# Performance work log

Hardware: AMD Instinct MI355X
Metric: run time of the kernel (lower is better)

Reference implementation:

```python
import jax, jax.numpy as jnp
import numpy as np

N = 50000
E = 800000
IN_C = 16
H = 64
EA = 3
L = 3
EPS = 1e-5

def layer_norm(h, g, b):
    mu = jnp.mean(h, axis=-1, keepdims=True)
    var = jnp.var(h, axis=-1, keepdims=True)
    return (h - mu) * jax.lax.rsqrt(var + EPS) * g + b

def setup_inputs() -> dict:
    key = jax.random.key(0)
    ks = jax.random.split(key, 24)
    s = lambda *sh: 0.05
    d = {}
    d["x"] = jax.random.normal(ks[0], (N, IN_C), jnp.float32)
    d["edge_index"] = jax.random.randint(ks[1], (2, E), 0, N, jnp.int32)
    d["edge_attr"] = jax.random.normal(ks[2], (E, EA), jnp.float32)
    # encoder
    d["enc_w"] = jax.random.normal(ks[3], (IN_C, H), jnp.float32) * 0.1
    d["enc_b"] = jnp.zeros((H,), jnp.float32)
    d["enc_ln_g"] = jnp.ones((H,), jnp.float32)
    d["enc_ln_b"] = jnp.zeros((H,), jnp.float32)
    # message-passing MLPs (stacked over layers)
    d["mlp_w1"] = jax.random.normal(ks[4], (L, H + EA, H // 2), jnp.float32) * 0.1
    d["mlp_b1"] = jnp.zeros((L, H // 2), jnp.float32)
    d["mlp_w2"] = jax.random.normal(ks[5], (L, H // 2, H), jnp.float32) * 0.1
    d["mlp_b2"] = jnp.zeros((L, H), jnp.float32)
    d["ln_g"] = jnp.ones((L, H), jnp.float32)
    d["ln_b"] = jnp.zeros((L, H), jnp.float32)
    # heads
    d["depth_w1"] = jax.random.normal(ks[6], (H, H // 2), jnp.float32) * 0.1
    d["depth_b1"] = jnp.zeros((H // 2,), jnp.float32)
    d["depth_w2"] = jax.random.normal(ks[7], (H // 2, 1), jnp.float32) * 0.1
    d["depth_b2"] = jnp.zeros((1,), jnp.float32)
    d["vel_w1"] = jax.random.normal(ks[8], (H, H // 2), jnp.float32) * 0.1
    d["vel_b1"] = jnp.zeros((H // 2,), jnp.float32)
    d["vel_w2"] = jax.random.normal(ks[9], (H // 2, 2), jnp.float32) * 0.1
    d["vel_b2"] = jnp.zeros((2,), jnp.float32)
    return d

def reference(x, edge_index, edge_attr, enc_w, enc_b, enc_ln_g, enc_ln_b,
              mlp_w1, mlp_b1, mlp_w2, mlp_b2, ln_g, ln_b,
              depth_w1, depth_b1, depth_w2, depth_b2,
              vel_w1, vel_b1, vel_w2, vel_b2):
    src, dst = edge_index[0], edge_index[1]  # PyG: x_j = x[src], aggregate at dst
    # encoder (dropout inactive in eval mode)
    h = layer_norm(x @ enc_w + enc_b, enc_ln_g, enc_ln_b)
    h = jax.nn.relu(h)
    # in-degree counts for mean aggregation (isolated nodes -> 0, like PyG)
    cnt = jax.ops.segment_sum(jnp.ones((E,), jnp.float32), dst, num_segments=N)
    inv_cnt = jnp.where(cnt > 0, 1.0 / jnp.maximum(cnt, 1.0), 0.0)[:, None]
    for i in range(L):
        m_in = jnp.concatenate([h[src], edge_attr], axis=1)          # [E, H+EA]
        m = jax.nn.relu(m_in @ mlp_w1[i] + mlp_b1[i]) @ mlp_w2[i] + mlp_b2[i]  # [E, H]
        agg = jax.ops.segment_sum(m, dst, num_segments=N) * inv_cnt  # mean aggregate
        h = layer_norm(h + agg, ln_g[i], ln_b[i])
    depth = jax.nn.relu(h @ depth_w1 + depth_b1) @ depth_w2 + depth_b2    # [N,1]
    velocity = jax.nn.relu(h @ vel_w1 + vel_b1) @ vel_w2 + vel_b2         # [N,2]
    return (depth, velocity)
```

## Files before the change

kernel.cpp:

```cpp
#include <hip/hip_runtime.h>
#include <hip/hip_bf16.h>

typedef __hip_bfloat16 bf16;
typedef unsigned int u32;
typedef float f4v __attribute__((ext_vector_type(4)));

#define NN 50000
#define NE 800000
#define INC 16
#define HD 64
#define EPSV 1e-5f
#define NB1 196

__device__ __forceinline__ float b2f(bf16 v) { return __bfloat162float(v); }
__device__ __forceinline__ bool is_bf(const void* det) {
  return *(const u32*)det == 0x3F803F80u;
}

__device__ __forceinline__ float4 ldnt4(const float4* p) {
  f4v t = __builtin_nontemporal_load(reinterpret_cast<const f4v*>(p));
  float4 r; r.x = t[0]; r.y = t[1]; r.z = t[2]; r.w = t[3];
  return r;
}

template<typename T> __device__ __forceinline__ float ldv(const T* p, int i);
template<> __device__ __forceinline__ float ldv<float>(const float* p, int i) { return p[i]; }
template<> __device__ __forceinline__ float ldv<bf16>(const bf16* p, int i) { return b2f(p[i]); }

#define W1F   0
#define B1F   6432
#define W2F   6528
#define B2F   12672
#define DW1F  12864
#define DB1F  14912
#define DW2F  14944
#define DB2F  14976
#define VW1F  14977
#define VB1F  17025
#define VW2F  17057
#define VB2F  17121
#define WFTOT 17123

#define H_OFF    0
#define P0_OFF   3200000
#define CSR_OFF  4800000
#define WF_OFF   8000000
#define CNTI_OFF (WF_OFF + WFTOT)
#define RS_OFF   (CNTI_OFF + NN)
#define BSUM_OFF (RS_OFF + NN)
#define BOFF_OFF (BSUM_OFF + 256)
#define LPOS_OFF (BOFF_OFF + 256)
#define INV_OFF  (LPOS_OFF + NE)
#define P1_OFF   (INV_OFF + NE)
#define WS_NEED_ROOMY ((size_t)(P1_OFF + NN * 32) * 4)

template<typename T>
__device__ __forceinline__ void prep_body(
    const T* w1, const T* b1, const T* w2, const T* b2,
    const T* dw1, const T* db1, const T* dw2, const T* db2,
    const T* vw1, const T* vb1, const T* vw2, const T* vb2,
    float* wf, int i) {
  float v;
  if      (i < B1F)  v = ldv(w1,  i - W1F);
  else if (i < W2F)  v = ldv(b1,  i - B1F);
  else if (i < B2F)  v = ldv(w2,  i - W2F);
  else if (i < DW1F) v = ldv(b2,  i - B2F);
  else if (i < DB1F) v = ldv(dw1, i - DW1F);
  else if (i < DW2F) v = ldv(db1, i - DB1F);
  else if (i < DB2F) v = ldv(dw2, i - DW2F);
  else if (i < VW1F) v = ldv(db2, i - DB2F);
  else if (i < VB1F) v = ldv(vw1, i - VW1F);
  else if (i < VW2F) v = ldv(vb1, i - VB1F);
  else if (i < VB2F) v = ldv(vw2, i - VW2F);
  else               v = ldv(vb2, i - VB2F);
  wf[i] = v;
}

__global__ __launch_bounds__(256) void prep_kernel(
    const void* w1, const void* b1, const void* w2, const void* b2,
    const void* dw1, const void* db1, const void* dw2, const void* db2,
    const void* vw1, const void* vb1, const void* vw2, const void* vb2,
    float* __restrict__ wf, const void* __restrict__ det) {
  int i = blockIdx.x * blockDim.x + threadIdx.x;
  if (i >= WFTOT) return;
  if (is_bf(det))
    prep_body((const bf16*)w1, (const bf16*)b1, (const bf16*)w2, (const bf16*)b2,
              (const bf16*)dw1, (const bf16*)db1, (const bf16*)dw2, (const bf16*)db2,
              (const bf16*)vw1, (const bf16*)vb1, (const bf16*)vw2, (const bf16*)vb2, wf, i);
  else
    prep_body((const float*)w1, (const float*)b1, (const float*)w2, (const float*)b2,
              (const float*)dw1, (const float*)db1, (const float*)dw2, (const float*)db2,
              (const float*)vw1, (const float*)vb1, (const float*)vw2, (const float*)vb2, wf, i);
}

__global__ __launch_bounds__(256) void encoder_kernel(
    const void* __restrict__ x, const void* __restrict__ enc_w,
    const void* __restrict__ enc_b, const void* __restrict__ g,
    const void* __restrict__ b, float* __restrict__ h,
    float* __restrict__ pout, const float* __restrict__ nw1,
    const float* __restrict__ nb1, const void* __restrict__ det) {
  __shared__ float shv[4][64];
  int node = (blockIdx.x * blockDim.x + threadIdx.x) >> 6;
  int lane = threadIdx.x & 63;
  int w = threadIdx.x >> 6;
  if (node >= NN) return;
  int jl = lane & 31, half = lane >> 5;
  float xv[INC], wv[INC], ebv, gv, bv;
  if (is_bf(det)) {
    const bf16* xp = (const bf16*)x + node * INC;
    const bf16* wp = (const bf16*)enc_w;
    #pragma unroll
    for (int k = 0; k < INC; k++) { xv[k] = b2f(xp[k]); wv[k] = b2f(wp[k * HD + lane]); }
    ebv = b2f(((const bf16*)enc_b)[lane]);
    gv  = b2f(((const bf16*)g)[lane]);
    bv  = b2f(((const bf16*)b)[lane]);
  } else {
    const float* xp = (const float*)x + node * INC;
    const float* wp = (const float*)enc_w;
    #pragma unroll
    for (int k = 0; k < INC; k++) { xv[k] = xp[k]; wv[k] = wp[k * HD + lane]; }
    ebv = ((const float*)enc_b)[lane];
    gv  = ((const float*)g)[lane];
    bv  = ((const float*)b)[lane];
  }
  float acc = ebv;
  #pragma unroll
  for (int k = 0; k < INC; k++) acc += xv[k] * wv[k];
  float s1 = acc, s2 = acc * acc;
  #pragma unroll
  for (int o = 32; o; o >>= 1) { s1 += __shfl_xor(s1, o); s2 += __shfl_xor(s2, o); }
  float mu = s1 * (1.0f / 64.0f);
  float var = fmaxf(s2 * (1.0f / 64.0f) - mu * mu, 0.0f);
  float d = acc - mu;
  float hv = fmaxf(d * rsqrtf(var + EPSV) * gv + bv, 0.0f);
  h[node * HD + lane] = hv;
  shv[w][lane] = hv;
  float pacc = 0.0f;
  int kb = half << 5;
  #pragma unroll
  for (int k4 = 0; k4 < 32; k4 += 4) {
    float4 h4 = *reinterpret_cast<const float4*>(&shv[w][kb + k4]);
    int kk = kb + k4;
    pacc += h4.x * nw1[kk * 32 + jl] + h4.y * nw1[(kk + 1) * 32 + jl]
          + h4.z * nw1[(kk + 2) * 32 + jl] + h4.w * nw1[(kk + 3) * 32 + jl];
  }
  pacc += __shfl_xor(pacc, 32);
  if (half == 0) pout[node * 32 + jl] = pacc + nb1[jl];
}

__global__ __launch_bounds__(256) void count_kernel(const int* __restrict__ ei,
                                                    int* __restrict__ cnt,
                                                    int* __restrict__ lpos) {
  int e = blockIdx.x * blockDim.x + threadIdx.x;
  if (e < NE) lpos[e] = atomicAdd(&cnt[ei[NE + e]], 1);
}

__global__ __launch_bounds__(256) void scan1_kernel(const int* __restrict__ cnt,
                                                    int* __restrict__ ex,
                                                    int* __restrict__ bsum) {
  __shared__ int s[256];
  int t = threadIdx.x, idx = blockIdx.x * 256 + t;
  int v = (idx < NN) ? cnt[idx] : 0;
  s[t] = v;
  __syncthreads();
  #pragma unroll
  for (int off = 1; off < 256; off <<= 1) {
    int u = (t >= off) ? s[t - off] : 0;
    __syncthreads();
    s[t] += u;
    __syncthreads();
  }
  if (idx < NN) ex[idx] = s[t] - v;
  if (t == 255) bsum[blockIdx.x] = s[255];
}

__global__ __launch_bounds__(256) void scan2_kernel(int* __restrict__ bsum,
                                                    int* __restrict__ boff) {
  __shared__ int s[256];
  int t = threadIdx.x;
  int v = (t < NB1) ? bsum[t] : 0;
  s[t] = v;
  __syncthreads();
  #pragma unroll
  for (int off = 1; off < 256; off <<= 1) {
    int u = (t >= off) ? s[t - off] : 0;
    __syncthreads();
    s[t] += u;
    __syncthreads();
  }
  boff[t] = s[t] - v;
}

__global__ __launch_bounds__(256) void scan3_kernel(int* __restrict__ rs,
                                                    const int* __restrict__ boff) {
  int idx = blockIdx.x * 256 + threadIdx.x;
  if (idx >= NN) return;
  rs[idx] += boff[blockIdx.x];
}

__global__ __launch_bounds__(256) void inv_kernel(const int* __restrict__ ei,
                                                  const int* __restrict__ rs,
                                                  const int* __restrict__ lpos,
                                                  int* __restrict__ inv) {
  int e = blockIdx.x * blockDim.x + threadIdx.x;
  if (e >= NE) return;
  int dst = ei[NE + e];
  inv[rs[dst] + lpos[e]] = e;
}

__global__ __launch_bounds__(256) void fill_kernel(const int* __restrict__ inv,
                                                   const int* __restrict__ ei,
                                                   const void* __restrict__ attr,
                                                   float4* __restrict__ csr,
                                                   const void* __restrict__ det) {
  int p = blockIdx.x * blockDim.x + threadIdx.x;
  if (p >= NE) return;
  int e = inv[p];
  int src = ei[e];
  float a0, a1, a2;
  if (is_bf(det)) {
    const bf16* ap = (const bf16*)attr + 3 * e;
    a0 = b2f(ap[0]); a1 = b2f(ap[1]); a2 = b2f(ap[2]);
  } else {
    const float* ap = (const float*)attr + 3 * e;
    a0 = ap[0]; a1 = ap[1]; a2 = ap[2];
  }
  float4 v; v.x = a0; v.y = a1; v.z = a2; v.w = __int_as_float(src);
  csr[p] = v;
}

__global__ __launch_bounds__(256) void node_pre_kernel(
    const float* __restrict__ h, const float* __restrict__ w1,
    const float* __restrict__ b1, float* __restrict__ p) {
  int t = blockIdx.x * blockDim.x + threadIdx.x;
  int node = t >> 5;
  int j = t & 31;
  if (node >= NN) return;
  const float* hr = h + node * HD;
  float acc = b1[j];
  #pragma unroll
  for (int k = 0; k < HD; k++) acc += hr[k] * w1[k * 32 + j];
  p[node * 32 + j] = acc;
}

__global__ __launch_bounds__(128) void gather_kernel(
    float* __restrict__ h, const float* __restrict__ pin,
    float* __restrict__ pnext, const float4* __restrict__ csr,
    const int* __restrict__ rs, const int* __restrict__ cnt,
    const float* __restrict__ w1a, const float* __restrict__ w2,
    const float* __restrict__ b2v, const void* __restrict__ gbase,
    const void* __restrict__ bbase, int layer,
    const float* __restrict__ nw1, const float* __restrict__ nb1,
    int do_pnext, const float* __restrict__ wf, void* __restrict__ out,
    const void* __restrict__ det) {
  __shared__ float sacc[2][2][32];
  __shared__ float shv[2][2][64];
  int wid = (blockIdx.x * blockDim.x + threadIdx.x) >> 6;
  int lane = threadIdx.x & 63;
  int w = threadIdx.x >> 6;
  int n0 = 2 * wid, n1 = 2 * wid + 1;
  if (n0 >= NN) return;
  int jl = lane & 31, half = lane >> 5;
  float wa0 = w1a[jl], wa1 = w1a[32 + jl], wa2 = w1a[64 + jl];
  int s0 = rs[n0], c0 = cnt[n0];
  int s1 = rs[n1], c1 = cnt[n1];
  float hres0 = h[n0 * HD + lane];
  float hres1 = h[n1 * HD + lane];
  float b2l = b2v[lane];

  bool isbf = is_bf(det);
  int gidx = layer * HD + lane;
  float gv, bv;
  if (isbf) {
    gv = b2f(((const bf16*)gbase)[gidx]);
    bv = b2f(((const bf16*)bbase)[gidx]);
  } else {
    gv = ((const float*)gbase)[gidx];
    bv = ((const float*)bbase)[gidx];
  }

  int cm10 = (c0 > 0) ? c0 - 1 : 0;
  int cm11 = (c1 > 0) ? c1 - 1 : 0;
  int t0 = (c0 > 0) ? s0 : 0;
  int t1 = (c1 > 0) ? s1 : 0;

  float acc0 = 0.0f, acc1 = 0.0f;
  int cmax = max(c0, c1);
  if (cmax > 0) {
    float4 ed0[8], ed1[8];
    #pragma unroll
    for (int t = 0; t < 8; t++) {
      ed0[t] = ldnt4(&csr[t0 + min(2 * t + half, cm10)]);
      ed1[t] = ldnt4(&csr[t1 + min(2 * t + half, cm11)]);
    }
    for (int b0 = 0; b0 < cmax; b0 += 16) {
      float q0[8], q1[8];
      #pragma unroll
      for (int t = 0; t < 8; t++) q0[t] = pin[__float_as_int(ed0[t].w) * 32 + jl];
      #pragma unroll
      for (int t = 0; t < 8; t++) q1[t] = pin[__float_as_int(ed1[t].w) * 32 + jl];
      float pa0[8], pa1[8];
      #pragma unroll
      for (int t = 0; t < 8; t++)
        pa0[t] = ed0[t].x * wa0 + ed0[t].y * wa1 + ed0[t].z * wa2;
      #pragma unroll
      for (int t = 0; t < 8; t++)
        pa1[t] = ed1[t].x * wa0 + ed1[t].y * wa1 + ed1[t].z * wa2;
      int nb = b0 + 16;
      if (nb < cmax) {
        #pragma unroll
        for (int t = 0; t < 8; t++) {
          ed0[t] = ldnt4(&csr[t0 + min(nb + 2 * t + half, cm10)]);
          ed1[t] = ldnt4(&csr[t1 + min(nb + 2 * t + half, cm11)]);
        }
      }
      #pragma unroll
      for (int t = 0; t < 8; t++) {
        int eoff = b0 + 2 * t + half;
        float r0v = fmaxf(q0[t] + pa0[t], 0.0f);
        acc0 += (eoff < c0) ? r0v : 0.0f;
        float r1v = fmaxf(q1[t] + pa1[t], 0.0f);
        acc1 += (eoff < c1) ? r1v : 0.0f;
      }
    }
  }
  acc0 += __shfl_xor(acc0, 32);
  acc1 += __shfl_xor(acc1, 32);

  if (half == 0) { sacc[w][0][jl] = acc0; sacc[w][1][jl] = acc1; }
  float m0 = 0.0f, m1 = 0.0f;
  #pragma unroll
  for (int j4 = 0; j4 < 32; j4 += 4) {
    float4 a0 = *reinterpret_cast<const float4*>(&sacc[w][0][j4]);
    float4 a1 = *reinterpret_cast<const float4*>(&sacc[w][1][j4]);
    float w20 = w2[(j4 + 0) * HD + lane], w21 = w2[(j4 + 1) * HD + lane];
    float w22 = w2[(j4 + 2) * HD + lane], w23 = w2[(j4 + 3) * HD + lane];
    m0 += a0.x * w20 + a0.y * w21 + a0.z * w22 + a0.w * w23;
    m1 += a1.x * w20 + a1.y * w21 + a1.z * w22 + a1.w * w23;
  }
  float aggv0 = (c0 > 0) ? (m0 / (float)c0 + b2l) : 0.0f;
  float aggv1 = (c1 > 0) ? (m1 / (float)c1 + b2l) : 0.0f;

  float v0 = hres0 + aggv0, v1 = hres1 + aggv1;
  float s10 = v0, s20 = v0 * v0, s11 = v1, s21 = v1 * v1;
  #pragma unroll
  for (int o = 32; o; o >>= 1) {
    s10 += __shfl_xor(s10, o); s20 += __shfl_xor(s20, o);
    s11 += __shfl_xor(s11, o); s21 += __shfl_xor(s21, o);
  }
  float mu0 = s10 * (1.0f / 64.0f), mu1 = s11 * (1.0f / 64.0f);
  float var0 = fmaxf(s20 * (1.0f / 64.0f) - mu0 * mu0, 0.0f);
  float var1 = fmaxf(s21 * (1.0f / 64.0f) - mu1 * mu1, 0.0f);
  float hv0 = (v0 - mu0) * rsqrtf(var0 + EPSV) * gv + bv;
  float hv1 = (v1 - mu1) * rsqrtf(var1 + EPSV) * gv + bv;

  shv[w][0][lane] = hv0;
  shv[w][1][lane] = hv1;

  if (do_pnext) {
    float p0a = 0.0f, p1a = 0.0f;
    int kb = half << 5;
    #pragma unroll
    for (int k4 = 0; k4 < 32; k4 += 4) {
      float4 h0 = *reinterpret_cast<const float4*>(&shv[w][0][kb + k4]);
      float4 h1 = *reinterpret_cast<const float4*>(&shv[w][1][kb + k4]);
      int kk = kb + k4;
      float n0v = nw1[kk * 32 + jl], n1v = nw1[(kk + 1) * 32 + jl];
      float n2v = nw1[(kk + 2) * 32 + jl], n3v = nw1[(kk + 3) * 32 + jl];
      p0a += h0.x * n0v + h0.y * n1v + h0.z * n2v + h0.w * n3v;
      p1a += h1.x * n0v + h1.y * n1v + h1.z * n2v + h1.w * n3v;
    }
    p0a += __shfl_xor(p0a, 32);
    p1a += __shfl_xor(p1a, 32);
    if (half == 0) {
      pnext[n0 * 32 + jl] = p0a + nb1[jl];
      pnext[n1 * 32 + jl] = p1a + nb1[jl];
    }
  }

  if (layer == 2) {
    const float* w1h = wf + (half ? VW1F : DW1F);
    float a20 = half ? wf[VB1F + jl] : wf[DB1F + jl];
    float a21 = a20;
    #pragma unroll
    for (int k4 = 0; k4 < 64; k4 += 4) {
      float4 h0 = *reinterpret_cast<const float4*>(&shv[w][0][k4]);
      float4 h1 = *reinterpret_cast<const float4*>(&shv[w][1][k4]);
      float wv0 = w1h[(k4 + 0) * 32 + jl], wv1 = w1h[(k4 + 1) * 32 + jl];
      float wv2 = w1h[(k4 + 2) * 32 + jl], wv3 = w1h[(k4 + 3) * 32 + jl];
      a20 += h0.x * wv0 + h0.y * wv1 + h0.z * wv2 + h0.w * wv3;
      a21 += h1.x * wv0 + h1.y * wv1 + h1.z * wv2 + h1.w * wv3;
    }
    a20 = fmaxf(a20, 0.0f);
    a21 = fmaxf(a21, 0.0f);
    float r00, r10, r01, r11;
    if (half == 0) {
      r00 = a20 * wf[DW2F + jl]; r10 = 0.0f;
      r01 = a21 * wf[DW2F + jl]; r11 = 0.0f;
    } else {
      r00 = a20 * wf[VW2F + 2 * jl]; r10 = a20 * wf[VW2F + 2 * jl + 1];
      r01 = a21 * wf[VW2F + 2 * jl]; r11 = a21 * wf[VW2F + 2 * jl + 1];
    }
    #pragma unroll
    for (int o = 16; o; o >>= 1) {
      r00 += __shfl_xor(r00, o); r10 += __shfl_xor(r10, o);
      r01 += __shfl_xor(r01, o); r11 += __shfl_xor(r11, o);
    }
    if (lane == 0) {
      float d0 = r00 + wf[DB2F];
      float d1 = r01 + wf[DB2F];
      if (isbf) {
        ((bf16*)out)[n0] = __float2bfloat16(d0);
        ((bf16*)out)[n1] = __float2bfloat16(d1);
      } else {
        ((float*)out)[n0] = d0;
        ((float*)out)[n1] = d1;
      }
    }
    if (lane == 32) {
      float v00 = r00 + wf[VB2F], v01 = r10 + wf[VB2F + 1];
      float v10 = r01 + wf[VB2F], v11 = r11 + wf[VB2F + 1];
      if (isbf) {
        ((bf16*)out)[NN + 2 * n0]     = __float2bfloat16(v00);
        ((bf16*)out)[NN + 2 * n0 + 1] = __float2bfloat16(v01);
        ((bf16*)out)[NN + 2 * n1]     = __float2bfloat16(v10);
        ((bf16*)out)[NN + 2 * n1 + 1] = __float2bfloat16(v11);
      } else {
        ((float*)out)[NN + 2 * n0]     = v00;
        ((float*)out)[NN + 2 * n0 + 1] = v01;
        ((float*)out)[NN + 2 * n1]     = v10;
        ((float*)out)[NN + 2 * n1 + 1] = v11;
      }
    }
  } else {
    h[n0 * HD + lane] = hv0;
    h[n1 * HD + lane] = hv1;
  }
}

extern "C" void kernel_launch(void* const* d_in, const int* in_sizes, int n_in,
                              void* d_out, int out_size, void* d_ws, size_t ws_size,
                              hipStream_t stream) {
  const void* x     = d_in[0];
  const int*  ei    = (const int*)d_in[1];
  const void* attr  = d_in[2];
  const void* enc_w = d_in[3];
  const void* enc_b = d_in[4];
  const void* enc_g = d_in[5];
  const void* enc_bb= d_in[6];
  const void* mw1   = d_in[7];
  const void* mb1   = d_in[8];
  const void* mw2   = d_in[9];
  const void* mb2   = d_in[10];
  const void* lng   = d_in[11];
  const void* lnb   = d_in[12];
  const void* dw1   = d_in[13];
  const void* db1   = d_in[14];
  const void* dw2   = d_in[15];
  const void* db2   = d_in[16];
  const void* vw1   = d_in[17];
  const void* vb1   = d_in[18];
  const void* vw2   = d_in[19];
  const void* vb2   = d_in[20];

  float* ws    = (float*)d_ws;
  float* h     = ws + H_OFF;
  float* p0    = ws + P0_OFF;
  float4* csr  = (float4*)(ws + CSR_OFF);
  float* wf    = ws + WF_OFF;
  int*   cnti  = (int*)(ws + CNTI_OFF);
  int*   rs    = (int*)(ws + RS_OFF);
  int*   bsum  = (int*)(ws + BSUM_OFF);
  int*   boff  = (int*)(ws + BOFF_OFF);
  int*   lpos  = (int*)(ws + LPOS_OFF);
  int*   inv   = (int*)(ws + INV_OFF);
  float* p1    = ws + P1_OFF;
  bool roomy = ws_size >= WS_NEED_ROOMY;

  hipMemsetAsync(cnti, 0, (size_t)NN * sizeof(int), stream);
  prep_kernel<<<(WFTOT + 255) / 256, 256, 0, stream>>>(
      mw1, mb1, mw2, mb2, dw1, db1, dw2, db2, vw1, vb1, vw2, vb2, wf, enc_g);
  encoder_kernel<<<(NN + 3) / 4, 256, 0, stream>>>(
      x, enc_w, enc_b, enc_g, enc_bb, h, p0, wf + W1F, wf + B1F, enc_g);
  count_kernel<<<(NE + 255) / 256, 256, 0, stream>>>(ei, cnti, lpos);
  scan1_kernel<<<NB1, 256, 0, stream>>>(cnti, rs, bsum);
  scan2_kernel<<<1, 256, 0, stream>>>(bsum, boff);
  scan3_kernel<<<NB1, 256, 0, stream>>>(rs, boff);
  inv_kernel<<<(NE + 255) / 256, 256, 0, stream>>>(ei, rs, lpos, inv);
  fill_kernel<<<(NE + 255) / 256, 256, 0, stream>>>(inv, ei, attr, csr, enc_g);

  for (int l = 0; l < 3; l++) {
    float* pin  = (roomy && (l & 1)) ? p1 : p0;
    float* pnxt = (roomy && !(l & 1)) ? p1 : p0;
    if (!roomy && l > 0) {
      node_pre_kernel<<<(NN * 32 + 255) / 256, 256, 0, stream>>>(
          h, wf + W1F + l * 2144, wf + B1F + l * 32, p0);
      pin = p0; pnxt = p0;
    }
    int do_pnext = (roomy && l < 2) ? 1 : 0;
    int nl = (l < 2) ? l + 1 : l;
    gather_kernel<<<(NN + 3) / 4, 128, 0, stream>>>(
        h, pin, pnxt, csr, rs, cnti,
        wf + W1F + l * 2144 + 64 * 32, wf + W2F + l * 2048, wf + B2F + l * 64,
        lng, lnb, l,
        wf + W1F + nl * 2144, wf + B1F + nl * 32, do_pnext,
        wf, d_out, enc_g);
  }
}
```

Measured before the change: 390.8 us.

## Store per-node pre-activations in fp16 and gather four edges per iteration

The per-node first-layer pre-activation tables are now stored as half precision instead of fp32, which halves the bytes moved by the random per-edge gather. Each lane now loads a half2 covering two features, so a 64-lane wave covers four edges per step instead of two. The edge prefetch and the cross-lane reductions are reorganised to match, with an extra shuffle stage. The risk is precision loss from fp16 rounding of intermediate activations.

```diff
diff --git a/kernel.cpp b/kernel.cpp
--- a/kernel.cpp
+++ b/kernel.cpp
@@ -1,5 +1,6 @@
 #include <hip/hip_runtime.h>
 #include <hip/hip_bf16.h>
+#include <hip/hip_fp16.h>
 
 typedef __hip_bfloat16 bf16;
 typedef unsigned int u32;
@@ -52,7 +53,7 @@
 #define LPOS_OFF (BOFF_OFF + 256)
 #define INV_OFF  (LPOS_OFF + NE)
 #define P1_OFF   (INV_OFF + NE)
-#define WS_NEED_ROOMY ((size_t)(P1_OFF + NN * 32) * 4)
+#define WS_NEED_ROOMY ((size_t)(P1_OFF + NN * 16) * 4)
 
 template<typename T>
 __device__ __forceinline__ void prep_body(
@@ -97,7 +98,7 @@
     const void* __restrict__ x, const void* __restrict__ enc_w,
     const void* __restrict__ enc_b, const void* __restrict__ g,
     const void* __restrict__ b, float* __restrict__ h,
-    float* __restrict__ pout, const float* __restrict__ nw1,
+    __half* __restrict__ pout, const float* __restrict__ nw1,
     const float* __restrict__ nb1, const void* __restrict__ det) {
   __shared__ float shv[4][64];
   int node = (blockIdx.x * blockDim.x + threadIdx.x) >> 6;
@@ -145,7 +146,7 @@
           + h4.z * nw1[(kk + 2) * 32 + jl] + h4.w * nw1[(kk + 3) * 32 + jl];
   }
   pacc += __shfl_xor(pacc, 32);
-  if (half == 0) pout[node * 32 + jl] = pacc + nb1[jl];
+  if (half == 0) pout[node * 32 + jl] = __float2half(pacc + nb1[jl]);
 }
 
 __global__ __launch_bounds__(256) void count_kernel(const int* __restrict__ ei,
@@ -231,7 +232,7 @@
 
 __global__ __launch_bounds__(256) void node_pre_kernel(
     const float* __restrict__ h, const float* __restrict__ w1,
-    const float* __restrict__ b1, float* __restrict__ p) {
+    const float* __restrict__ b1, __half* __restrict__ p) {
   int t = blockIdx.x * blockDim.x + threadIdx.x;
   int node = t >> 5;
   int j = t & 31;
@@ -240,12 +241,12 @@
   float acc = b1[j];
   #pragma unroll
   for (int k = 0; k < HD; k++) acc += hr[k] * w1[k * 32 + j];
-  p[node * 32 + j] = acc;
+  p[node * 32 + j] = __float2half(acc);
 }
 
 __global__ __launch_bounds__(128) void gather_kernel(
-    float* __restrict__ h, const float* __restrict__ pin,
-    float* __restrict__ pnext, const float4* __restrict__ csr,
+    float* __restrict__ h, const __half2* __restrict__ pin,
+    __half* __restrict__ pnext, const float4* __restrict__ csr,
     const int* __restrict__ rs, const int* __restrict__ cnt,
     const float* __restrict__ w1a, const float* __restrict__ w2,
     const float* __restrict__ b2v, const void* __restrict__ gbase,
@@ -261,7 +262,10 @@
   int n0 = 2 * wid, n1 = 2 * wid + 1;
   if (n0 >= NN) return;
   int jl = lane & 31, half = lane >> 5;
-  float wa0 = w1a[jl], wa1 = w1a[32 + jl], wa2 = w1a[64 + jl];
+  int q4 = lane >> 4, pp = lane & 15;
+  float2 wa0 = *reinterpret_cast<const float2*>(&w1a[2 * pp]);
+  float2 wa1 = *reinterpret_cast<const float2*>(&w1a[32 + 2 * pp]);
+  float2 wa2 = *reinterpret_cast<const float2*>(&w1a[64 + 2 * pp]);
   int s0 = rs[n0], c0 = cnt[n0];
   int s1 = rs[n1], c1 = cnt[n1];
   float hres0 = h[n0 * HD + lane];
@@ -284,50 +288,62 @@
   int t0 = (c0 > 0) ? s0 : 0;
   int t1 = (c1 > 0) ? s1 : 0;
 
-  float acc0 = 0.0f, acc1 = 0.0f;
+  float2 acc0 = make_float2(0.f, 0.f), acc1 = make_float2(0.f, 0.f);
   int cmax = max(c0, c1);
   if (cmax > 0) {
-    float4 ed0[8], ed1[8];
+    float4 e0[4], e1[4];
     #pragma unroll
-    for (int t = 0; t < 8; t++) {
-      ed0[t] = ldnt4(&csr[t0 + min(2 * t + half, cm10)]);
-      ed1[t] = ldnt4(&csr[t1 + min(2 * t + half, cm11)]);
+    for (int t = 0; t < 4; t++) {
+      e0[t] = ldnt4(&csr[t0 + min(4 * t + q4, cm10)]);
+      e1[t] = ldnt4(&csr[t1 + min(4 * t + q4, cm11)]);
     }
     for (int b0 = 0; b0 < cmax; b0 += 16) {
-      float q0[8], q1[8];
+      float2 g0[4], g1[4];
       #pragma unroll
-      for (int t = 0; t < 8; t++) q0[t] = pin[__float_as_int(ed0[t].w) * 32 + jl];
+      for (int t = 0; t < 4; t++)
+        g0[t] = __half22float2(pin[__float_as_int(e0[t].w) * 16 + pp]);
       #pragma unroll
-      for (int t = 0; t < 8; t++) q1[t] = pin[__float_as_int(ed1[t].w) * 32 + jl];
-      float pa0[8], pa1[8];
+      for (int t = 0; t < 4; t++)
+        g1[t] = __half22float2(pin[__float_as_int(e1[t].w) * 16 + pp]);
+      float2 pa0[4], pa1[4];
       #pragma unroll
-      for (int t = 0; t < 8; t++)
-        pa0[t] = ed0[t].x * wa0 + ed0[t].y * wa1 + ed0[t].z * wa2;
-      #pragma unroll
-      for (int t = 0; t < 8; t++)
-        pa1[t] = ed1[t].x * wa0 + ed1[t].y * wa1 + ed1[t].z * wa2;
+      for (int t = 0; t < 4; t++) {
+        pa0[t].x = e0[t].x * wa0.x + e0[t].y * wa1.x + e0[t].z * wa2.x;
+        pa0[t].y = e0[t].x * wa0.y + e0[t].y * wa1.y + e0[t].z * wa2.y;
+        pa1[t].x = e1[t].x * wa0.x + e1[t].y * wa1.x + e1[t].z * wa2.x;
+        pa1[t].y = e1[t].x * wa0.y + e1[t].y * wa1.y + e1[t].z * wa2.y;
+      }
       int nb = b0 + 16;
       if (nb < cmax) {
         #pragma unroll
-        for (int t = 0; t < 8; t++) {
-          ed0[t] = ldnt4(&csr[t0 + min(nb + 2 * t + half, cm10)]);
-          ed1[t] = ldnt4(&csr[t1 + min(nb + 2 * t + half, cm11)]);
+        for (int t = 0; t < 4; t++) {
+          e0[t] = ldnt4(&csr[t0 + min(nb + 4 * t + q4, cm10)]);
+          e1[t] = ldnt4(&csr[t1 + min(nb + 4 * t + q4, cm11)]);
         }
       }
       #pragma unroll
-      for (int t = 0; t < 8; t++) {
-        int eoff = b0 + 2 * t + half;
-        float r0v = fmaxf(q0[t] + pa0[t], 0.0f);
-        acc0 += (eoff < c0) ? r0v : 0.0f;
-        float r1v = fmaxf(q1[t] + pa1[t], 0.0f);
-        acc1 += (eoff < c1) ? r1v : 0.0f;
+      for (int t = 0; t < 4; t++) {
+        int eo = b0 + 4 * t + q4;
+        float rx0 = fmaxf(g0[t].x + pa0[t].x, 0.0f);
+        float ry0 = fmaxf(g0[t].y + pa0[t].y, 0.0f);
+        acc0.x += (eo < c0) ? rx0 : 0.0f;
+        acc0.y += (eo < c0) ? ry0 : 0.0f;
+        float rx1 = fmaxf(g1[t].x + pa1[t].x, 0.0f);
+        float ry1 = fmaxf(g1[t].y + pa1[t].y, 0.0f);
+        acc1.x += (eo < c1) ? rx1 : 0.0f;
+        acc1.y += (eo < c1) ? ry1 : 0.0f;
       }
     }
   }
-  acc0 += __shfl_xor(acc0, 32);
-  acc1 += __shfl_xor(acc1, 32);
-
-  if (half == 0) { sacc[w][0][jl] = acc0; sacc[w][1][jl] = acc1; }
+  acc0.x += __shfl_xor(acc0.x, 16); acc0.y += __shfl_xor(acc0.y, 16);
+  acc1.x += __shfl_xor(acc1.x, 16); acc1.y += __shfl_xor(acc1.y, 16);
+  acc0.x += __shfl_xor(acc0.x, 32); acc0.y += __shfl_xor(acc0.y, 32);
+  acc1.x += __shfl_xor(acc1.x, 32); acc1.y += __shfl_xor(acc1.y, 32);
+  if (lane < 16) {
+    *reinterpret_cast<float2*>(&sacc[w][0][2 * pp]) = acc0;
+    *reinterpret_cast<float2*>(&sacc[w][1][2 * pp]) = acc1;
+  }
+
   float m0 = 0.0f, m1 = 0.0f;
   #pragma unroll
   for (int j4 = 0; j4 < 32; j4 += 4) {
@@ -373,8 +389,8 @@
     p0a += __shfl_xor(p0a, 32);
     p1a += __shfl_xor(p1a, 32);
     if (half == 0) {
-      pnext[n0 * 32 + jl] = p0a + nb1[jl];
-      pnext[n1 * 32 + jl] = p1a + nb1[jl];
+      pnext[n0 * 32 + jl] = __float2half(p0a + nb1[jl]);
+      pnext[n1 * 32 + jl] = __float2half(p1a + nb1[jl]);
     }
   }
 
@@ -465,7 +481,7 @@
 
   float* ws    = (float*)d_ws;
   float* h     = ws + H_OFF;
-  float* p0    = ws + P0_OFF;
+  __half* p0   = (__half*)(ws + P0_OFF);
   float4* csr  = (float4*)(ws + CSR_OFF);
   float* wf    = ws + WF_OFF;
   int*   cnti  = (int*)(ws + CNTI_OFF);
@@ -474,7 +490,7 @@
   int*   boff  = (int*)(ws + BOFF_OFF);
   int*   lpos  = (int*)(ws + LPOS_OFF);
   int*   inv   = (int*)(ws + INV_OFF);
-  float* p1    = ws + P1_OFF;
+  __half* p1   = (__half*)(ws + P1_OFF);
   bool roomy = ws_size >= WS_NEED_ROOMY;
 
   hipMemsetAsync(cnti, 0, (size_t)NN * sizeof(int), stream);
@@ -490,8 +506,8 @@
   fill_kernel<<<(NE + 255) / 256, 256, 0, stream>>>(inv, ei, attr, csr, enc_g);
 
   for (int l = 0; l < 3; l++) {
-    float* pin  = (roomy && (l & 1)) ? p1 : p0;
-    float* pnxt = (roomy && !(l & 1)) ? p1 : p0;
+    __half* pin  = (roomy && (l & 1)) ? p1 : p0;
+    __half* pnxt = (roomy && !(l & 1)) ? p1 : p0;
     if (!roomy && l > 0) {
       node_pre_kernel<<<(NN * 32 + 255) / 256, 256, 0, stream>>>(
           h, wf + W1F + l * 2144, wf + B1F + l * 32, p0);
@@ -500,7 +516,7 @@
     int do_pnext = (roomy && l < 2) ? 1 : 0;
     int nl = (l < 2) ? l + 1 : l;
     gather_kernel<<<(NN + 3) / 4, 128, 0, stream>>>(
-        h, pin, pnxt, csr, rs, cnti,
+        h, (const __half2*)pin, pnxt, csr, rs, cnti,
         wf + W1F + l * 2144 + 64 * 32, wf + W2F + l * 2048, wf + B2F + l * 64,
         lng, lnb, l,
         wf + W1F + nl * 2144, wf + B1F + nl * 32, do_pnext,
```

Result: faster. 344.9 us (-11.7%).
